# Performance work log

Measured on AMD Instinct MI355X. Metric: run time of the kernel, lower is better.

## Reference

```python
import jax, jax.numpy as jnp
import numpy as np

B, S, D, H = 8, 2048, 768, 768


def setup_inputs() -> dict:
    key = jax.random.key(0)
    kx, kq, kk, kv = jax.random.split(key, 4)
    scale = 1.0 / np.sqrt(D)
    return {
        "x": jax.random.normal(kx, (B, S, D), dtype=jnp.float32),
        "Wq": jax.random.normal(kq, (D, H), dtype=jnp.float32) * scale,
        "Wk": jax.random.normal(kk, (D, H), dtype=jnp.float32) * scale,
        "Wv": jax.random.normal(kv, (D, H), dtype=jnp.float32) * scale,
    }


def reference(x, Wq, Wk, Wv):
    # Dense(use_bias=False) projections
    q = jnp.einsum("bsd,dh->bsh", x, Wq)
    k = jnp.einsum("bsd,dh->bsh", x, Wk)
    v = jnp.einsum("bsd,dh->bsh", x, Wv)
    S_len = x.shape[-2]
    # NOTE: source does NOT scale by 1/sqrt(head_size)
    scores = jnp.einsum("bqh,bkh->bqk", q, k)  # [B, S, S]
    tril = jnp.tril(jnp.ones((S_len, S_len), dtype=jnp.float32))
    scores = jnp.where(tril == 0, -jnp.inf, scores)
    attn = jax.nn.softmax(scores, axis=-1)
    # Dropout rate is 0.0 in Config -> identity
    return jnp.einsum("bqk,bkh->bqh", attn, v)
```

## Files before the change

kernel.cpp:

```cpp
#include <hip/hip_runtime.h>

typedef unsigned short u16;
typedef _Float16 f16;
typedef float  f32x4  __attribute__((ext_vector_type(4)));
typedef unsigned short u16x4 __attribute__((ext_vector_type(4)));
typedef f16    f16x8  __attribute__((ext_vector_type(8)));

__device__ __forceinline__ u16 f2h(float f) {
  f16 h = (f16)f;
  return __builtin_bit_cast(u16, h);
}

#define BARRIER()                          \
  do {                                     \
    asm volatile("" ::: "memory");         \
    __builtin_amdgcn_s_barrier();          \
    asm volatile("" ::: "memory");         \
  } while (0)

template <int N> __device__ __forceinline__ void vmwait() {
  if constexpr (N == 0)       asm volatile("s_waitcnt vmcnt(0)" ::: "memory");
  else if constexpr (N == 3)  asm volatile("s_waitcnt vmcnt(3)" ::: "memory");
  else if constexpr (N == 4)  asm volatile("s_waitcnt vmcnt(4)" ::: "memory");
  else if constexpr (N == 5)  asm volatile("s_waitcnt vmcnt(5)" ::: "memory");
  else if constexpr (N == 6)  asm volatile("s_waitcnt vmcnt(6)" ::: "memory");
  else if constexpr (N == 8)  asm volatile("s_waitcnt vmcnt(8)" ::: "memory");
  else if constexpr (N == 10) asm volatile("s_waitcnt vmcnt(10)" ::: "memory");
}

#define GLL16(g, l)                                                              \
  __builtin_amdgcn_global_load_lds(                                              \
      (const __attribute__((address_space(1))) unsigned int*)(g),                \
      (__attribute__((address_space(3))) unsigned int*)(l), 16, 0, 0)

__global__ __launch_bounds__(256) void prep_kernel(
    const float* __restrict__ x, const float* __restrict__ Wq,
    const float* __restrict__ Wk, const float* __restrict__ Wv,
    u16* __restrict__ xf, u16* __restrict__ wq16,
    u16* __restrict__ wk16, u16* __restrict__ wvt16) {
  const int bid = blockIdx.x, tid = threadIdx.x;
  if (bid < 13440) {
    const float* src;
    u16* dst;
    int i;
    if (bid < 12288) { src = x;  dst = xf;   i = bid * 256 + tid; }
    else if (bid < 12864) { src = Wq; dst = wq16; i = (bid - 12288) * 256 + tid; }
    else { src = Wk; dst = wk16; i = (bid - 12864) * 256 + tid; }
    f32x4 v = ((const f32x4*)src)[i];
    u16x4 h;
#pragma unroll
    for (int j = 0; j < 4; ++j) h[j] = f2h(v[j]);
    ((u16x4*)dst)[i] = h;
  } else {
    int i = (bid - 13440) * 256 + tid;
    int h = i / 768, d = i % 768;
    wvt16[i] = f2h(Wv[d * 768 + h]);
  }
}

template <int EPI, int CAUSAL, int KROW, int BM, int BN, int DEPTH>
__device__ __forceinline__ void gemm_body(
    u16* __restrict__ lds,
    const u16* __restrict__ pA, const u16* __restrict__ pB,
    void* __restrict__ Cv, size_t cbase,
    int K, int lda, int ldb, int ldc, int ti, int tj) {
  constexpr int ASZ = BM * 32;
  constexpr int BSZ = BN * 32;
  u16* As = lds;
  u16* Bs = lds + DEPTH * ASZ;

  const int t = threadIdx.x, w = t >> 6, l = t & 63;
  const int wr = w >> 1, wc = w & 1;
  const int lr = l & 15, lk = l >> 4;
  constexpr int MI = BM / 32;
  constexpr int NI = BN / 32;
  constexpr int LPS = BM / 64 + BN / 64;

  const int srow = t >> 2;
  const int sk8 = ((t & 3) ^ ((srow >> 1) & 3)) * 8;
  const int ck = ((lk ^ ((lr >> 1) & 3)) << 3);

  const int Keff = KROW ? (ti + 1) * BM : K;
  const int nsteps = Keff >> 5;

  auto stage = [&](int bu, int kk) {
    const int kb = kk * 32;
#pragma unroll
    for (int s = 0; s < BM / 64; ++s)
      GLL16(pA + (size_t)(ti * BM + s * 64 + srow) * lda + sk8 + kb,
            As + bu * ASZ + s * 2048 + w * 512);
#pragma unroll
    for (int s = 0; s < BN / 64; ++s)
      GLL16(pB + (size_t)(tj * BN + s * 64 + srow) * ldb + sk8 + kb,
            Bs + bu * BSZ + s * 2048 + w * 512);
  };

  f32x4 acc[MI][NI] = {};

  stage(0, 0);
  if constexpr (DEPTH == 3) { if (nsteps > 1) stage(1, 1); }
  for (int kk = 0; kk < nsteps; ++kk) {
    const int buf = kk % DEPTH;
    if constexpr (DEPTH == 2) {
      if (kk + 1 < nsteps) { stage((kk + 1) % 2, kk + 1); vmwait<LPS>(); }
      else vmwait<0>();
    } else {
      if (kk + 2 < nsteps) { stage((kk + 2) % 3, kk + 2); vmwait<2 * LPS>(); }
      else if (kk + 1 < nsteps) vmwait<LPS>();
      else vmwait<0>();
    }
    BARRIER();

    f16x8 ah[MI], bh[NI];
#pragma unroll
    for (int mi = 0; mi < MI; ++mi) {
      const int ae = buf * ASZ + (wr * (BM / 2) + mi * 16 + lr) * 32 + ck;
      ah[mi] = *(const f16x8*)&As[ae];
    }
#pragma unroll
    for (int ni = 0; ni < NI; ++ni) {
      const int be = buf * BSZ + (wc * (BN / 2) + ni * 16 + lr) * 32 + ck;
      bh[ni] = *(const f16x8*)&Bs[be];
    }
#pragma unroll
    for (int mi = 0; mi < MI; ++mi)
#pragma unroll
      for (int ni = 0; ni < NI; ++ni)
        acc[mi][ni] = __builtin_amdgcn_mfma_f32_16x16x32_f16(ah[mi], bh[ni], acc[mi][ni], 0, 0, 0);
    BARRIER();
  }

#pragma unroll
  for (int mi = 0; mi < MI; ++mi)
#pragma unroll
    for (int ni = 0; ni < NI; ++ni)
#pragma unroll
      for (int r = 0; r < 4; ++r) {
        const int row = ti * BM + wr * (BM / 2) + mi * 16 + lk * 4 + r;
        const int col = tj * BN + wc * (BN / 2) + ni * 16 + lr;
        float v = acc[mi][ni][r];
        if (CAUSAL && col > row) v = -1e30f;
        const size_t idx = cbase + (size_t)row * ldc + col;
        if (EPI == 0) ((float*)Cv)[idx] = v;
        else          ((u16*)Cv)[idx] = f2h(v);
      }
}

template <int EPI, int CAUSAL, int BM, int BN, int DEPTH, int MINW>
__global__ __launch_bounds__(256, MINW) void gemm_k(
    const u16* __restrict__ A, long sAb, const u16* __restrict__ B, long sBb,
    void* __restrict__ Cv, long sCb,
    int K, int lda, int ldb, int ldc, int gx, int gy) {
  __shared__ __align__(16) u16 lds[DEPTH * (BM * 32 + BN * 32)];
  const int nwg = gridDim.x;
  const int orig = blockIdx.x;
  const int q8 = nwg >> 3, r8 = nwg & 7;
  const int xcd = orig & 7, pos = orig >> 3;
  const int wgid = (xcd < r8 ? xcd * (q8 + 1) : r8 * (q8 + 1) + (xcd - r8) * q8) + pos;
  const int tj = wgid % gx;
  const int rest = wgid / gx;
  const int ti = rest % gy;
  const int zb = rest / gy;
  if (CAUSAL && tj > ti) return;
  gemm_body<EPI, CAUSAL, 0, BM, BN, DEPTH>(
      lds, A + (size_t)zb * sAb, B + (size_t)zb * sBb,
      Cv, (size_t)zb * sCb, K, lda, ldb, ldc, ti, tj);
}

__global__ __launch_bounds__(256, 3) void proj_kernel(
    const u16* __restrict__ xf, const u16* __restrict__ mt16,
    const u16* __restrict__ wvt16,
    u16* __restrict__ qf, u16* __restrict__ vtf) {
  __shared__ __align__(16) u16 lds[20480];
  const int orig = blockIdx.x;
  const int wgid = (orig & 7) * 96 + (orig >> 3);
  gemm_body<2, 0, 0, 64, 256, 2>(lds, xf, mt16, qf, 0,
                                 768, 768, 768, 768, wgid / 3, wgid % 3);
  gemm_body<2, 0, 0, 128, 128, 2>(lds, wvt16, xf, vtf, 0,
                                  768, 768, 768, 16384, wgid % 6, wgid / 6);
}

__global__ __launch_bounds__(256, 3) void pv_kernel(
    const u16* __restrict__ P, long sPb,
    const u16* __restrict__ vt,
    float* __restrict__ out, long sOb) {
  __shared__ __align__(16) u16 lds[20480];
  const int orig = blockIdx.x;
  const int nwg = gridDim.x;
  const int wgid = (orig & 7) * (nwg >> 3) + (orig >> 3);
  const int tj = wgid % 3;
  const int s5 = (wgid / 3) % 32;
  const int zb = wgid / 96;
  const int ti = (s5 & 1) ? (s5 >> 1) : (31 - (s5 >> 1));
  gemm_body<0, 0, 1, 64, 256, 2>(
      lds, P + (size_t)zb * sPb, vt + (size_t)zb * 2048,
      out, (size_t)zb * sOb, 2048, 2048, 16384, 768, ti, tj);
}

__global__ __launch_bounds__(256) void softmax_kernel(const float* __restrict__ S,
                                                      u16* __restrict__ P,
                                                      long sSb, long sPb) {
  const int wid = blockIdx.x * 4 + (threadIdx.x >> 6);
  const int l = threadIdx.x & 63;
  const int zb = wid >> 11;
  const int i = wid & 2047;
  const float* row = S + (size_t)zb * sSb + (size_t)i * 2048;
  u16* prow = P + (size_t)zb * sPb + (size_t)i * 2048;
  const int Tend = ((i >> 7) + 1) << 7;
  const int nch = (Tend + 255) >> 8;

  f32x4 vb[8];
  float mx = -3e38f;
  for (int c = 0; c < nch; ++c) {
    const int j = c * 256 + l * 4;
    f32x4 v;
    if (j < Tend) v = *(const f32x4*)(row + j);
    else { v[0] = v[1] = v[2] = v[3] = -3e38f; }
    vb[c] = v;
    mx = fmaxf(mx, fmaxf(fmaxf(v[0], v[1]), fmaxf(v[2], v[3])));
  }
#pragma unroll
  for (int s = 32; s; s >>= 1) mx = fmaxf(mx, __shfl_xor(mx, s));

  float sum = 0.f;
  for (int c = 0; c < nch; ++c) {
    f32x4 v = vb[c];
#pragma unroll
    for (int j = 0; j < 4; ++j) {
      float e = expf(v[j] - mx);
      v[j] = e;
      sum += e;
    }
    vb[c] = v;
  }
#pragma unroll
  for (int s = 32; s; s >>= 1) sum += __shfl_xor(sum, s);
  const float inv = 1.f / sum;

  for (int c = 0; c < nch; ++c) {
    const int j = c * 256 + l * 4;
    if (j < Tend) {
      f32x4 v = vb[c];
      u16x4 o;
#pragma unroll
      for (int q = 0; q < 4; ++q) o[q] = f2h(v[q] * inv);
      *(u16x4*)(prow + j) = o;
    }
  }
}

extern "C" void kernel_launch(void* const* d_in, const int* in_sizes, int n_in,
                              void* d_out, int out_size, void* d_ws, size_t ws_size,
                              hipStream_t stream) {
  const float* x  = (const float*)d_in[0];
  const float* Wq = (const float*)d_in[1];
  const float* Wk = (const float*)d_in[2];
  const float* Wv = (const float*)d_in[3];
  float* out = (float*)d_out;

  const int S = 2048, D = 768;
  const size_t ND = (size_t)8 * S * D;
  const size_t NW = (size_t)D * D;

  char* ws = (char*)d_ws;
  size_t off = 0;
  auto alloc = [&](size_t bytes) { size_t o = off; off = (off + bytes + 255) & ~(size_t)255; return o; };

  u16* xf   = (u16*)(ws + alloc(ND * 2));
  u16* qf   = (u16*)(ws + alloc(ND * 2));
  u16* vtf  = (u16*)(ws + alloc(ND * 2));
  u16* wq16 = (u16*)(ws + alloc(NW * 2));
  u16* wk16 = (u16*)(ws + alloc(NW * 2));
  u16* wvt16= (u16*)(ws + alloc(NW * 2));
  u16* mt16 = (u16*)(ws + alloc(NW * 2));
  const size_t fixed = off;

  const size_t perBatch = (size_t)S * S * 4 + (size_t)S * S * 2 + 512;
  int g = 0;
  for (int cand = 8; cand >= 1; cand >>= 1)
    if (fixed + (size_t)cand * perBatch <= ws_size) { g = cand; break; }
  if (!g) return;

  float* sc = (float*)(ws + alloc((size_t)g * S * S * 4));
  u16*   P  = (u16*)(ws + alloc((size_t)g * S * S * 2));

  prep_kernel<<<15744, 256, 0, stream>>>(x, Wq, Wk, Wv, xf, wq16, wk16, wvt16);

  gemm_k<2, 0, 128, 64, 2, 4><<<72, 256, 0, stream>>>(
      wk16, 0, wq16, 0, mt16, 0, 768, 768, 768, 768, 12, 6);

  proj_kernel<<<768, 256, 0, stream>>>(xf, mt16, wvt16, qf, vtf);

  for (int b0 = 0; b0 < 8; b0 += g) {
    gemm_k<0, 1, 128, 128, 2, 4><<<16 * 16 * g, 256, 0, stream>>>(
        qf + (size_t)b0 * S * D, (long)S * D,
        xf + (size_t)b0 * S * D, (long)S * D,
        sc, (long)S * S, 768, 768, 768, 2048, 16, 16);

    softmax_kernel<<<g * 512, 256, 0, stream>>>(sc, P, (long)S * S, (long)S * S);

    pv_kernel<<<96 * g, 256, 0, stream>>>(
        P, (long)S * S, vtf + (size_t)b0 * S,
        out + (size_t)b0 * S * D, (long)S * D);
  }
}
```

Measured before the change: 242.6 us.

## Use LDS-tiled Wv transpose and uniform 128x128 triple-buffered tiles in proj/pv

The Wv transpose in the prep kernel now goes through a padded 64x64 shared-memory tile, so both the read and the write are coalesced instead of strided scalar gathers. The projection kernel becomes two 128x128 jobs per workgroup interleaving Q and V^T tiles, and both the projection and PV GEMMs move to 128x128 tiles with three-stage LDS buffering. The aim is better global access, data reuse and latency hiding, at the cost of more LDS per workgroup, which could lower occupancy, and a different tile-to-workgroup mapping in PV.

```diff
diff --git a/kernel.cpp b/kernel.cpp
--- a/kernel.cpp
+++ b/kernel.cpp
@@ -38,6 +38,7 @@
     const float* __restrict__ Wk, const float* __restrict__ Wv,
     u16* __restrict__ xf, u16* __restrict__ wq16,
     u16* __restrict__ wk16, u16* __restrict__ wvt16) {
+  __shared__ float tlds[64][65];
   const int bid = blockIdx.x, tid = threadIdx.x;
   if (bid < 13440) {
     const float* src;
@@ -52,9 +53,20 @@
     for (int j = 0; j < 4; ++j) h[j] = f2h(v[j]);
     ((u16x4*)dst)[i] = h;
   } else {
-    int i = (bid - 13440) * 256 + tid;
-    int h = i / 768, d = i % 768;
-    wvt16[i] = f2h(Wv[d * 768 + h]);
+    const int tb = bid - 13440;
+    const int d0 = (tb / 12) * 64, h0 = (tb % 12) * 64;
+    const int c = tid & 63, grp = tid >> 6;
+#pragma unroll
+    for (int r = 0; r < 16; ++r) {
+      const int dd = grp * 16 + r;
+      tlds[dd][c] = Wv[(size_t)(d0 + dd) * 768 + h0 + c];
+    }
+    __syncthreads();
+#pragma unroll
+    for (int r = 0; r < 16; ++r) {
+      const int hh = grp * 16 + r;
+      wvt16[(size_t)(h0 + hh) * 768 + d0 + c] = f2h(tlds[c][hh]);
+    }
   }
 }
 
@@ -171,28 +183,36 @@
     const u16* __restrict__ xf, const u16* __restrict__ mt16,
     const u16* __restrict__ wvt16,
     u16* __restrict__ qf, u16* __restrict__ vtf) {
-  __shared__ __align__(16) u16 lds[20480];
+  __shared__ __align__(16) u16 lds[3 * (4096 + 4096)];
   const int orig = blockIdx.x;
   const int wgid = (orig & 7) * 96 + (orig >> 3);
-  gemm_body<2, 0, 0, 64, 256, 2>(lds, xf, mt16, qf, 0,
-                                 768, 768, 768, 768, wgid / 3, wgid % 3);
-  gemm_body<2, 0, 0, 128, 128, 2>(lds, wvt16, xf, vtf, 0,
-                                  768, 768, 768, 16384, wgid % 6, wgid / 6);
+#pragma unroll
+  for (int j = 0; j < 2; ++j) {
+    const int job = wgid * 2 + j;
+    const int sidx = job / 12, sub = job % 12;
+    if (sub < 6) {
+      gemm_body<2, 0, 0, 128, 128, 3>(lds, xf, mt16, qf, 0,
+                                      768, 768, 768, 768, sidx, sub);
+    } else {
+      gemm_body<2, 0, 0, 128, 128, 3>(lds, wvt16, xf, vtf, 0,
+                                      768, 768, 768, 16384, sub - 6, sidx);
+    }
+  }
 }
 
 __global__ __launch_bounds__(256, 3) void pv_kernel(
     const u16* __restrict__ P, long sPb,
     const u16* __restrict__ vt,
     float* __restrict__ out, long sOb) {
-  __shared__ __align__(16) u16 lds[20480];
+  __shared__ __align__(16) u16 lds[3 * (4096 + 4096)];
   const int orig = blockIdx.x;
   const int nwg = gridDim.x;
   const int wgid = (orig & 7) * (nwg >> 3) + (orig >> 3);
-  const int tj = wgid % 3;
-  const int s5 = (wgid / 3) % 32;
+  const int tj = wgid % 6;
+  const int s = (wgid / 6) % 16;
   const int zb = wgid / 96;
-  const int ti = (s5 & 1) ? (s5 >> 1) : (31 - (s5 >> 1));
-  gemm_body<0, 0, 1, 64, 256, 2>(
+  const int ti = (s & 1) ? (s >> 1) : (15 - (s >> 1));
+  gemm_body<0, 0, 1, 128, 128, 3>(
       lds, P + (size_t)zb * sPb, vt + (size_t)zb * 2048,
       out, (size_t)zb * sOb, 2048, 2048, 16384, 768, ti, tj);
 }
@@ -284,7 +304,7 @@
   float* sc = (float*)(ws + alloc((size_t)g * S * S * 4));
   u16*   P  = (u16*)(ws + alloc((size_t)g * S * S * 2));
 
-  prep_kernel<<<15744, 256, 0, stream>>>(x, Wq, Wk, Wv, xf, wq16, wk16, wvt16);
+  prep_kernel<<<13584, 256, 0, stream>>>(x, Wq, Wk, Wv, xf, wq16, wk16, wvt16);
 
   gemm_k<2, 0, 128, 64, 2, 4><<<72, 256, 0, stream>>>(
       wk16, 0, wq16, 0, mt16, 0, 768, 768, 768, 768, 12, 6);
```

Result: faster. 225.2 us (-7.2%).
